# Optimization experiments

Measured on AMD Instinct MI355X. Metric: run time of the kernel, lower is better.

The kernel has to match this reference:

```python
import jax, jax.numpy as jnp
import numpy as np

EPS = 1e-9
NUM_GATES = 64
SECOND_THRESHOLD = 0.2  # eval threshold (module defaults train==eval)
CAPACITY_FACTOR = 1.25
MIN_EXPERT_CAPACITY = 4


def setup_inputs() -> dict:
    key = jax.random.key(0)
    k1, k2, k3 = jax.random.split(key, 3)
    b, n, d = 8, 2048, 1024
    x = jax.random.normal(k1, (b, n, d), dtype=jnp.float32)
    w_gating = jax.random.normal(k2, (d, NUM_GATES), dtype=jnp.float32)
    uniform_noise = jax.random.uniform(k3, (b, n), dtype=jnp.float32)
    return {"x": x, "w_gating": w_gating, "uniform_noise": uniform_noise}


def reference(x, w_gating, uniform_noise):
    b, n, d = x.shape
    e = NUM_GATES
    dt = x.dtype

    # raw gates: small matmul + softmax over experts
    raw_gates = jax.nn.softmax(jnp.einsum('bnd,de->bne', x, w_gating), axis=-1)

    # top-1 expert
    gate_1 = jnp.max(raw_gates, axis=-1)            # [b, n]
    index_1 = jnp.argmax(raw_gates, axis=-1)        # [b, n]
    mask_1 = jax.nn.one_hot(index_1, e, dtype=dt)   # [b, n, e]
    density_1_proxy = raw_gates

    # top-2 expert (top-1 of gates with top-1 removed)
    gates_wo1 = raw_gates * (1.0 - mask_1)
    gate_2 = jnp.max(gates_wo1, axis=-1)
    index_2 = jnp.argmax(gates_wo1, axis=-1)
    mask_2 = jax.nn.one_hot(index_2, e, dtype=dt)

    # renormalize top-2 gate values
    denom = gate_1 + gate_2 + EPS
    gate_1 = gate_1 / denom
    gate_2 = gate_2 / denom

    # load-balancing loss
    density_1 = jnp.mean(mask_1, axis=-2)                 # [b, e]
    loss = jnp.mean(jnp.mean(density_1_proxy, axis=-2) * density_1) * float(e * e)

    # second policy == 'random': route to 2nd expert with prob ~ gate_2 / threshold
    keep2 = (uniform_noise < (gate_2 / max(SECOND_THRESHOLD, EPS))).astype(dt)
    mask_2 = mask_2 * keep2[..., None]

    # static expert capacity
    cap = max(min(n, int((n * 2) / e * CAPACITY_FACTOR)), MIN_EXPERT_CAPACITY)
    capf = float(cap)

    # exclusive cumsum over tokens -> position of each token within its expert
    pos1 = (jnp.cumsum(mask_1, axis=-2) - mask_1) * mask_1        # [b, n, e]
    mask_1 = mask_1 * (pos1 < capf).astype(dt)
    mask_1_count = jnp.sum(mask_1, axis=-2, keepdims=True)        # [b, 1, e]
    mask_1_flat = jnp.sum(mask_1, axis=-1)                        # [b, n]
    pos1 = jnpp_sum = jnp.sum(pos1, axis=-1)                      # [b, n]
    gate_1 = gate_1 * mask_1_flat

    pos2 = (jnp.cumsum(mask_2, axis=-2) - mask_2) + mask_1_count
    pos2 = pos2 * mask_2
    mask_2 = mask_2 * (pos2 < capf).astype(dt)
    mask_2_flat = jnp.sum(mask_2, axis=-1)
    pos2 = jnp.sum(pos2, axis=-1)
    gate_2 = gate_2 * mask_2_flat

    # combine tensor [b, n, e, cap]; out-of-range positions one-hot to zero
    oh_e1 = jax.nn.one_hot(index_1, e, dtype=dt)
    oh_e2 = jax.nn.one_hot(index_2, e, dtype=dt)
    oh_c1 = jax.nn.one_hot(pos1.astype(jnp.int32), cap, dtype=dt)
    oh_c2 = jax.nn.one_hot(pos2.astype(jnp.int32), cap, dtype=dt)
    combine = (gate_1[..., None, None] * oh_e1[..., :, None] * oh_c1[..., None, :]
               + gate_2[..., None, None] * oh_e2[..., :, None] * oh_c2[..., None, :])
    dispatch = (combine > 0).astype(dt)
    return dispatch, combine, loss
```

## Files before the change

### kernel.cpp

```cpp
#include <hip/hip_runtime.h>
#include <math.h>

#define NTOK 16384
#define NPB  2048
#define DDIM 1024
#define NEXP 64
#define CAP  80
#define ROWF 5120
#define SOUT 83886080LL

typedef float vf4 __attribute__((ext_vector_type(4)));

#define OFF_ROUTE  0
#define OFF_POS1   (OFF_ROUTE + NTOK*4)
#define OFF_POS2   (OFF_POS1  + NTOK*4)
#define OFF_CNT1   (OFF_POS2  + NTOK*4)
#define OFF_PART   (OFF_CNT1  + 2048)
#define OFF_G12    (OFF_PART  + 131072)

__global__ __launch_bounds__(256) void k_gate(
    const float* __restrict__ x, const float* __restrict__ w,
    const float* __restrict__ noise,
    int* __restrict__ route, float2* __restrict__ g12,
    float* __restrict__ part)
{
    __shared__ float xs[32][34];
    __shared__ float wl[32][64];
    __shared__ float lg[32][68];
    __shared__ float sG[4][64];

    const int tid  = threadIdx.x;
    const int tok0 = blockIdx.x * 32;
    const int tx = tid & 15, ty = tid >> 4;
    float acc[2][4] = {{0.f}};

    const float* xb = x + (size_t)tok0 * DDIM;

    for (int k0 = 0; k0 < DDIM; k0 += 32) {
        {
            int t = tid >> 3, c = tid & 7;
            float4 v = *(const float4*)(xb + (size_t)t * DDIM + k0 + 4 * c);
            xs[4*c+0][t] = v.x; xs[4*c+1][t] = v.y;
            xs[4*c+2][t] = v.z; xs[4*c+3][t] = v.w;
            const float4* wp = (const float4*)(w + (size_t)k0 * NEXP);
            ((float4*)wl)[tid]       = wp[tid];
            ((float4*)wl)[tid + 256] = wp[tid + 256];
        }
        __syncthreads();
        #pragma unroll
        for (int k = 0; k < 32; ++k) {
            float2 a  = *(const float2*)&xs[k][ty * 2];
            float4 bb = *(const float4*)&wl[k][tx * 4];
            float av[2] = {a.x, a.y};
            float bv[4] = {bb.x, bb.y, bb.z, bb.w};
            #pragma unroll
            for (int i = 0; i < 2; ++i)
                #pragma unroll
                for (int j = 0; j < 4; ++j)
                    acc[i][j] = fmaf(av[i], bv[j], acc[i][j]);
        }
        __syncthreads();
    }

    #pragma unroll
    for (int i = 0; i < 2; ++i)
        #pragma unroll
        for (int j = 0; j < 4; ++j)
            lg[ty * 2 + i][tx * 4 + j] = acc[i][j];
    __syncthreads();

    const int lane = tid & 63;
    const int wv   = tid >> 6;
    float gsum_acc = 0.f;

    for (int it = 0; it < 8; ++it) {
        int t = wv * 8 + it;
        float v = lg[t][lane];

        float m = v; int mi = lane;
        #pragma unroll
        for (int off = 32; off; off >>= 1) {
            float ov = __shfl_xor(m, off, 64);
            int   oi = __shfl_xor(mi, off, 64);
            if (ov > m || (ov == m && oi < mi)) { m = ov; mi = oi; }
        }
        float v2 = (lane == mi) ? -INFINITY : v;
        float m2 = v2; int mi2 = lane;
        #pragma unroll
        for (int off = 32; off; off >>= 1) {
            float ov = __shfl_xor(m2, off, 64);
            int   oi = __shfl_xor(mi2, off, 64);
            if (ov > m2 || (ov == m2 && oi < mi2)) { m2 = ov; mi2 = oi; }
        }
        float ex = expf(v - m);
        float s = ex;
        #pragma unroll
        for (int off = 32; off; off >>= 1) s += __shfl_xor(s, off, 64);

        float inv   = 1.0f / s;
        float gate1 = inv;
        float gate2 = expf(m2 - m) * inv;
        gsum_acc += ex * inv;

        float denom = gate1 + gate2 + 1e-9f;
        float g1n = gate1 / denom;
        float g2n = gate2 / denom;

        int gt = tok0 + t;
        if (lane == 0) {
            float u = noise[gt];
            int k2 = (u < (g2n / 0.2f)) ? 1 : 0;
            route[gt] = mi | (mi2 << 8) | (k2 << 16);
            g12[gt] = make_float2(g1n, g2n);
        }
    }

    sG[wv][lane] = gsum_acc;
    __syncthreads();
    if (tid < 64)
        part[blockIdx.x * 64 + tid] =
            sG[0][tid] + sG[1][tid] + sG[2][tid] + sG[3][tid];
}

__global__ __launch_bounds__(64) void k_pos(
    const int* __restrict__ route,
    int* __restrict__ pos1, int* __restrict__ pos2raw,
    int* __restrict__ cnt1tot)
{
    const int b = blockIdx.x;
    const int e = threadIdx.x;
    __shared__ int sr[64];
    int c1 = 0, c2 = 0;
    const int base = b * NPB;
    int nxt = route[base + e];
    for (int c0 = 0; c0 < NPB; c0 += 64) {
        sr[e] = nxt;
        __syncthreads();
        if (c0 + 64 < NPB) nxt = route[base + c0 + 64 + e];
        #pragma unroll 8
        for (int j = 0; j < 64; ++j) {
            int r = sr[j];
            if ((r & 255) == e) { pos1[base + c0 + j] = c1; c1++; }
            if ((r >> 16) && ((r >> 8) & 255) == e) { pos2raw[base + c0 + j] = c2; c2++; }
        }
        __syncthreads();
    }
    cnt1tot[b * NEXP + e] = c1;
}

__global__ __launch_bounds__(256) void k_out(
    const int* __restrict__ route,
    const int* __restrict__ pos1, const int* __restrict__ pos2raw,
    const int* __restrict__ cnt1tot,
    const float2* __restrict__ g12, const float* __restrict__ part,
    float* __restrict__ out)
{
    const int tid = threadIdx.x;
    const int bid = blockIdx.x;

    if (bid == 4096) {
        __shared__ float red[4];
        float v = 0.f;
        for (int p = tid; p < 512; p += 256) {
            int b = p >> 6, e = p & 63;
            float s = 0.f;
            for (int c = 0; c < 64; ++c) s += part[((b << 6) + c) * 64 + e];
            v += s * (float)cnt1tot[p];
        }
        #pragma unroll
        for (int off = 32; off; off >>= 1) v += __shfl_xor(v, off, 64);
        if ((tid & 63) == 0) red[tid >> 6] = v;
        __syncthreads();
        if (tid == 0)
            out[2 * SOUT] = (red[0] + red[1] + red[2] + red[3]) * (1.0f / 524288.0f);
        return;
    }

    const int tg = bid * 4;

    __shared__ int   se[4][2];
    __shared__ float sv[4][2];

    if (tid < 4) {
        int t = tg + tid;
        int b = t >> 11;
        int r  = route[t];
        int i1 = r & 255, i2 = (r >> 8) & 255, k2 = (r >> 16);
        float2 g = g12[t];

        int p1 = pos1[t];
        se[tid][0] = (p1 < CAP) ? (i1 * CAP + p1) : -1;
        sv[tid][0] = g.x;

        int e2 = -1;
        if (k2) {
            int m1c = min(cnt1tot[(b << 6) + i2], CAP);
            int p2  = pos2raw[t] + m1c;
            if (p2 < CAP) e2 = i2 * CAP + p2;
        }
        se[tid][1] = e2;
        sv[tid][1] = g.y;
    }
    __syncthreads();

    vf4* dbase = (vf4*)(out + (size_t)tg * ROWF);
    vf4* cbase = (vf4*)(out + (size_t)SOUT + (size_t)tg * ROWF);
    #pragma unroll
    for (int t = 0; t < 4; ++t) {
        const int   e1 = se[t][0], e2 = se[t][1];
        const float v1 = sv[t][0], v2 = sv[t][1];
        vf4* pd = dbase + (size_t)t * (ROWF / 4);
        vf4* pc = cbase + (size_t)t * (ROWF / 4);
        for (int s = tid; s < ROWF / 4; s += 256) {
            int b4 = s * 4;
            bool a0 = (b4     == e1), b0 = (b4     == e2);
            bool a1 = (b4 + 1 == e1), b1 = (b4 + 1 == e2);
            bool a2 = (b4 + 2 == e1), b2 = (b4 + 2 == e2);
            bool a3 = (b4 + 3 == e1), b3 = (b4 + 3 == e2);
            vf4 c, d;
            c.x = a0 ? v1 : (b0 ? v2 : 0.f);  d.x = (a0 | b0) ? 1.f : 0.f;
            c.y = a1 ? v1 : (b1 ? v2 : 0.f);  d.y = (a1 | b1) ? 1.f : 0.f;
            c.z = a2 ? v1 : (b2 ? v2 : 0.f);  d.z = (a2 | b2) ? 1.f : 0.f;
            c.w = a3 ? v1 : (b3 ? v2 : 0.f);  d.w = (a3 | b3) ? 1.f : 0.f;
            __builtin_nontemporal_store(d, pd + s);
            __builtin_nontemporal_store(c, pc + s);
        }
    }
}

extern "C" void kernel_launch(void* const* d_in, const int* in_sizes, int n_in,
                              void* d_out, int out_size, void* d_ws, size_t ws_size,
                              hipStream_t stream) {
    (void)in_sizes; (void)n_in; (void)ws_size; (void)out_size;
    const float* x     = (const float*)d_in[0];
    const float* w     = (const float*)d_in[1];
    const float* noise = (const float*)d_in[2];
    float* out = (float*)d_out;
    char*  ws  = (char*)d_ws;

    int*    route   = (int*)   (ws + OFF_ROUTE);
    int*    pos1    = (int*)   (ws + OFF_POS1);
    int*    pos2raw = (int*)   (ws + OFF_POS2);
    int*    cnt1tot = (int*)   (ws + OFF_CNT1);
    float*  part    = (float*) (ws + OFF_PART);
    float2* g12     = (float2*)(ws + OFF_G12);

    k_gate<<<dim3(NTOK / 32), dim3(256), 0, stream>>>(
        x, w, noise, route, g12, part);
    k_pos<<<dim3(8), dim3(64), 0, stream>>>(
        route, pos1, pos2raw, cnt1tot);
    k_out<<<dim3(4097), dim3(256), 0, stream>>>(
        route, pos1, pos2raw, cnt1tot, g12, part, out);
}
```

Before: 903.1 us.

## Enlarge gating tile with register prefetch, parallelize position scan, simplify output fill

The gating matmul now processes 64 tokens per block with a 4x4 register tile and prefetches the next x/w slice into registers before the compute loop. This raises reuse of the w tile and hides global load latency. The position kernel changes from a 64-thread serial scan to a 256-thread two-pass chunked histogram plus prefix scan, which cuts the serial latency of that stage. The output fill uses a single quad-index comparison per store instead of eight element comparisons, and the loss reduction is adjusted to 32 partials per batch. Halving the gating grid to 256 blocks may lower occupancy on a large GPU.

```diff
diff --git a/kernel.cpp b/kernel.cpp
--- a/kernel.cpp
+++ b/kernel.cpp
@@ -16,7 +16,7 @@
 #define OFF_POS2   (OFF_POS1  + NTOK*4)
 #define OFF_CNT1   (OFF_POS2  + NTOK*4)
 #define OFF_PART   (OFF_CNT1  + 2048)
-#define OFF_G12    (OFF_PART  + 131072)
+#define OFF_G12    (OFF_PART  + 65536)
 
 __global__ __launch_bounds__(256) void k_gate(
     const float* __restrict__ x, const float* __restrict__ w,
@@ -24,37 +24,49 @@
     int* __restrict__ route, float2* __restrict__ g12,
     float* __restrict__ part)
 {
-    __shared__ float xs[32][34];
+    __shared__ float xs[32][68];
     __shared__ float wl[32][64];
-    __shared__ float lg[32][68];
+    __shared__ float lg[64][68];
     __shared__ float sG[4][64];
 
     const int tid  = threadIdx.x;
-    const int tok0 = blockIdx.x * 32;
+    const int tok0 = blockIdx.x * 64;
     const int tx = tid & 15, ty = tid >> 4;
-    float acc[2][4] = {{0.f}};
+    float acc[4][4] = {{0.f}};
 
     const float* xb = x + (size_t)tok0 * DDIM;
+    const int t0 = tid >> 3, c0 = (tid & 7) * 4;
+
+    float4 px0 = *(const float4*)(xb + (size_t)t0 * DDIM + c0);
+    float4 px1 = *(const float4*)(xb + (size_t)(t0 + 32) * DDIM + c0);
+    float4 pw0 = ((const float4*)w)[tid];
+    float4 pw1 = ((const float4*)w)[tid + 256];
 
     for (int k0 = 0; k0 < DDIM; k0 += 32) {
-        {
-            int t = tid >> 3, c = tid & 7;
-            float4 v = *(const float4*)(xb + (size_t)t * DDIM + k0 + 4 * c);
-            xs[4*c+0][t] = v.x; xs[4*c+1][t] = v.y;
-            xs[4*c+2][t] = v.z; xs[4*c+3][t] = v.w;
-            const float4* wp = (const float4*)(w + (size_t)k0 * NEXP);
-            ((float4*)wl)[tid]       = wp[tid];
-            ((float4*)wl)[tid + 256] = wp[tid + 256];
-        }
+        xs[c0+0][t0] = px0.x; xs[c0+1][t0] = px0.y;
+        xs[c0+2][t0] = px0.z; xs[c0+3][t0] = px0.w;
+        xs[c0+0][t0+32] = px1.x; xs[c0+1][t0+32] = px1.y;
+        xs[c0+2][t0+32] = px1.z; xs[c0+3][t0+32] = px1.w;
+        ((float4*)wl)[tid]       = pw0;
+        ((float4*)wl)[tid + 256] = pw1;
         __syncthreads();
+
+        if (k0 + 32 < DDIM) {
+            px0 = *(const float4*)(xb + (size_t)t0 * DDIM + k0 + 32 + c0);
+            px1 = *(const float4*)(xb + (size_t)(t0 + 32) * DDIM + k0 + 32 + c0);
+            const float4* wp = (const float4*)(w + (size_t)(k0 + 32) * NEXP);
+            pw0 = wp[tid];
+            pw1 = wp[tid + 256];
+        }
+
         #pragma unroll
         for (int k = 0; k < 32; ++k) {
-            float2 a  = *(const float2*)&xs[k][ty * 2];
+            float4 a  = *(const float4*)&xs[k][ty * 4];
             float4 bb = *(const float4*)&wl[k][tx * 4];
-            float av[2] = {a.x, a.y};
+            float av[4] = {a.x, a.y, a.z, a.w};
             float bv[4] = {bb.x, bb.y, bb.z, bb.w};
             #pragma unroll
-            for (int i = 0; i < 2; ++i)
+            for (int i = 0; i < 4; ++i)
                 #pragma unroll
                 for (int j = 0; j < 4; ++j)
                     acc[i][j] = fmaf(av[i], bv[j], acc[i][j]);
@@ -63,18 +75,17 @@
     }
 
     #pragma unroll
-    for (int i = 0; i < 2; ++i)
-        #pragma unroll
-        for (int j = 0; j < 4; ++j)
-            lg[ty * 2 + i][tx * 4 + j] = acc[i][j];
+    for (int i = 0; i < 4; ++i)
+        *(float4*)&lg[ty * 4 + i][tx * 4] =
+            make_float4(acc[i][0], acc[i][1], acc[i][2], acc[i][3]);
     __syncthreads();
 
     const int lane = tid & 63;
     const int wv   = tid >> 6;
     float gsum_acc = 0.f;
 
-    for (int it = 0; it < 8; ++it) {
-        int t = wv * 8 + it;
+    for (int it = 0; it < 16; ++it) {
+        int t = wv * 16 + it;
         float v = lg[t][lane];
 
         float m = v; int mi = lane;
@@ -122,30 +133,60 @@
             sG[0][tid] + sG[1][tid] + sG[2][tid] + sG[3][tid];
 }
 
-__global__ __launch_bounds__(64) void k_pos(
+__global__ __launch_bounds__(256) void k_pos(
     const int* __restrict__ route,
     int* __restrict__ pos1, int* __restrict__ pos2raw,
     int* __restrict__ cnt1tot)
 {
-    const int b = blockIdx.x;
-    const int e = threadIdx.x;
-    __shared__ int sr[64];
-    int c1 = 0, c2 = 0;
-    const int base = b * NPB;
-    int nxt = route[base + e];
-    for (int c0 = 0; c0 < NPB; c0 += 64) {
-        sr[e] = nxt;
-        __syncthreads();
-        if (c0 + 64 < NPB) nxt = route[base + c0 + 64 + e];
+    const int b    = blockIdx.x;
+    const int tid  = threadIdx.x;
+    const int lane = tid & 63, wv = tid >> 6;
+    __shared__ int sr[NPB];
+    __shared__ int h1[32][64], h2[32][64];
+
+    for (int i = tid; i < NPB; i += 256) sr[i] = route[b * NPB + i];
+    __syncthreads();
+
+    for (int tau = wv; tau < 32; tau += 4) {
+        int c1 = 0, c2 = 0;
+        const int* p = &sr[tau * 64];
         #pragma unroll 8
         for (int j = 0; j < 64; ++j) {
-            int r = sr[j];
-            if ((r & 255) == e) { pos1[base + c0 + j] = c1; c1++; }
-            if ((r >> 16) && ((r >> 8) & 255) == e) { pos2raw[base + c0 + j] = c2; c2++; }
-        }
-        __syncthreads();
-    }
-    cnt1tot[b * NEXP + e] = c1;
+            int r = p[j];
+            c1 += ((r & 255) == lane);
+            c2 += ((r >> 16) && (((r >> 8) & 255) == lane));
+        }
+        h1[tau][lane] = c1; h2[tau][lane] = c2;
+    }
+    __syncthreads();
+
+    if (tid < 64) {
+        int run = 0;
+        #pragma unroll 8
+        for (int tau = 0; tau < 32; ++tau) {
+            int t = h1[tau][tid]; h1[tau][tid] = run; run += t;
+        }
+        cnt1tot[b * NEXP + tid] = run;
+    } else if (tid < 128) {
+        int e = tid - 64, run = 0;
+        #pragma unroll 8
+        for (int tau = 0; tau < 32; ++tau) {
+            int t = h2[tau][e]; h2[tau][e] = run; run += t;
+        }
+    }
+    __syncthreads();
+
+    for (int tau = wv; tau < 32; tau += 4) {
+        int c1 = h1[tau][lane], c2 = h2[tau][lane];
+        const int* p = &sr[tau * 64];
+        const int gbase = b * NPB + tau * 64;
+        #pragma unroll 4
+        for (int j = 0; j < 64; ++j) {
+            int r = p[j];
+            if ((r & 255) == lane) pos1[gbase + j] = c1++;
+            if ((r >> 16) && (((r >> 8) & 255) == lane)) pos2raw[gbase + j] = c2++;
+        }
+    }
 }
 
 __global__ __launch_bounds__(256) void k_out(
@@ -164,7 +205,8 @@
         for (int p = tid; p < 512; p += 256) {
             int b = p >> 6, e = p & 63;
             float s = 0.f;
-            for (int c = 0; c < 64; ++c) s += part[((b << 6) + c) * 64 + e];
+            #pragma unroll 8
+            for (int c = 0; c < 32; ++c) s += part[((b << 5) + c) * 64 + e];
             v += s * (float)cnt1tot[p];
         }
         #pragma unroll
@@ -209,19 +251,14 @@
     for (int t = 0; t < 4; ++t) {
         const int   e1 = se[t][0], e2 = se[t][1];
         const float v1 = sv[t][0], v2 = sv[t][1];
+        const int   q1 = e1 >> 2, q2 = e2 >> 2;
         vf4* pd = dbase + (size_t)t * (ROWF / 4);
         vf4* pc = cbase + (size_t)t * (ROWF / 4);
         for (int s = tid; s < ROWF / 4; s += 256) {
-            int b4 = s * 4;
-            bool a0 = (b4     == e1), b0 = (b4     == e2);
-            bool a1 = (b4 + 1 == e1), b1 = (b4 + 1 == e2);
-            bool a2 = (b4 + 2 == e1), b2 = (b4 + 2 == e2);
-            bool a3 = (b4 + 3 == e1), b3 = (b4 + 3 == e2);
-            vf4 c, d;
-            c.x = a0 ? v1 : (b0 ? v2 : 0.f);  d.x = (a0 | b0) ? 1.f : 0.f;
-            c.y = a1 ? v1 : (b1 ? v2 : 0.f);  d.y = (a1 | b1) ? 1.f : 0.f;
-            c.z = a2 ? v1 : (b2 ? v2 : 0.f);  d.z = (a2 | b2) ? 1.f : 0.f;
-            c.w = a3 ? v1 : (b3 ? v2 : 0.f);  d.w = (a3 | b3) ? 1.f : 0.f;
+            vf4 d = {0.f, 0.f, 0.f, 0.f};
+            vf4 c = {0.f, 0.f, 0.f, 0.f};
+            if (s == q1) { d[e1 & 3] = 1.f; c[e1 & 3] = v1; }
+            if (s == q2) { d[e2 & 3] = 1.f; c[e2 & 3] = v2; }
             __builtin_nontemporal_store(d, pd + s);
             __builtin_nontemporal_store(c, pc + s);
         }
@@ -245,9 +282,9 @@
     float*  part    = (float*) (ws + OFF_PART);
     float2* g12     = (float2*)(ws + OFF_G12);
 
-    k_gate<<<dim3(NTOK / 32), dim3(256), 0, stream>>>(
+    k_gate<<<dim3(NTOK / 64), dim3(256), 0, stream>>>(
         x, w, noise, route, g12, part);
-    k_pos<<<dim3(8), dim3(64), 0, stream>>>(
+    k_pos<<<dim3(8), dim3(256), 0, stream>>>(
         route, pos1, pos2raw, cnt1tot);
     k_out<<<dim3(4097), dim3(256), 0, stream>>>(
         route, pos1, pos2raw, cnt1tot, g12, part, out);
```

Result: faster. 800.4 us (-11.4%).
